# Performance work log

Measured on AMD Instinct MI355X. Metric: run time of the kernel, lower is better.

The kernel has to match this reference:

```python
import jax, jax.numpy as jnp
import numpy as np

NEG_INF = -jnp.inf

def _sage_conv(x_src, x_dst, src, dst, Wl, bl, Wr, aggr, num_nodes):
    # messages = source features gathered along edges  [E, d]
    msgs = x_src[src]
    if aggr == 'mean':
        s = jax.ops.segment_sum(msgs, dst, num_segments=num_nodes)
        cnt = jax.ops.segment_sum(jnp.ones((src.shape[0],), x_src.dtype), dst, num_segments=num_nodes)
        agg = s / jnp.maximum(cnt, 1.0)[:, None]
    else:  # max; isolated targets -> 0 (PyG scatter-max fill)
        m = jax.ops.segment_max(msgs, dst, num_segments=num_nodes)
        agg = jnp.where(jnp.isfinite(m), m, 0.0)
    return agg @ Wl.T + bl + x_dst @ Wr.T

def setup_inputs() -> dict:
    key = jax.random.key(0)
    ks = jax.random.split(key, 12)
    N, E, D, H, C, L = 40000, 640000, 128, 128, 64, 2
    sc = 0.05
    return {
        'x': jax.random.normal(ks[0], (N, D), jnp.float32),
        'edge_index0': jax.random.randint(ks[1], (2, E), 0, N, jnp.int64),
        'edge_index1': jax.random.randint(ks[2], (2, E), 0, N, jnp.int64),
        'Wl_mean': jax.random.normal(ks[3], (L, H, D), jnp.float32) * sc,
        'bl_mean': jax.random.normal(ks[4], (L, H), jnp.float32) * sc,
        'Wr_mean': jax.random.normal(ks[5], (L, H, D), jnp.float32) * sc,
        'Wl_max': jax.random.normal(ks[6], (L, H, D), jnp.float32) * sc,
        'bl_max': jax.random.normal(ks[7], (L, H), jnp.float32) * sc,
        'Wr_max': jax.random.normal(ks[8], (L, H, D), jnp.float32) * sc,
        'post_W': jax.random.normal(ks[9], (C, 2 * L * H), jnp.float32) * sc,
        'post_b': jax.random.normal(ks[10], (C,), jnp.float32) * sc,
    }

def reference(x, edge_index0, edge_index1, Wl_mean, bl_mean, Wr_mean, Wl_max, bl_max, Wr_max, post_W, post_b):
    N = x.shape[0]
    edge_sets = [edge_index0, edge_index1]
    L = len(edge_sets)
    h = x
    all_layers = []
    for i, ei in enumerate(edge_sets):
        src, dst = ei[0], ei[1]
        x_mean = _sage_conv(h, h, src, dst, Wl_mean[i], bl_mean[i], Wr_mean[i], 'mean', N)
        x_max = _sage_conv(h, h, src, dst, Wl_max[i], bl_max[i], Wr_max[i], 'max', N)
        all_layers.append(x_mean)
        all_layers.append(x_max)
        if i != L - 1:
            h = jax.nn.relu(h)  # note: original never replaces x with conv output
    x_final = jnp.concatenate(all_layers, axis=1) @ post_W.T + post_b
    return jax.nn.log_softmax(x_final, axis=-1)
```

## Files before the change

### kernel.cpp

```cpp
#include <hip/hip_runtime.h>
#include <cstdint>
#include <cstddef>

constexpr int FD = 128;
constexpr int CC = 64;
constexpr int KTOT = 768;
constexpr int CAP = 48;
constexpr int SS = 4096;

typedef __attribute__((ext_vector_type(8))) short short8;
typedef __attribute__((ext_vector_type(4))) float f32x4;

__device__ __forceinline__ float u2f(unsigned u) {
  union { unsigned u; float f; } v; v.u = u; return v.f;
}
__device__ __forceinline__ unsigned f2bf(float f) {
  union { float f; unsigned u; } v; v.f = f;
  return (v.u + 0x7FFFu + ((v.u >> 16) & 1u)) >> 16;
}
__device__ __forceinline__ unsigned pack2(float a, float b) {
  return f2bf(a) | (f2bf(b) << 16);
}
__device__ __forceinline__ unsigned relu_pk(unsigned v) {
  unsigned m = ((v >> 15) & 0x10001u) * 0xFFFFu;
  return v & ~m;
}

__global__ __launch_bounds__(256) void initpre_kernel(
    const float* __restrict__ x, uint4* __restrict__ xbf4, uint4* __restrict__ xrbf4,
    int n8, int* __restrict__ cnt, int ncnt,
    const float* __restrict__ Wl_mean, const float* __restrict__ bl_mean,
    const float* __restrict__ Wr_mean, const float* __restrict__ Wl_max,
    const float* __restrict__ bl_max,  const float* __restrict__ Wr_max,
    const float* __restrict__ postW,   const float* __restrict__ postb,
    unsigned short* __restrict__ Mbf, float* __restrict__ cb)
{
  const int gtid = blockIdx.x * 256 + threadIdx.x;
  const int gsz = gridDim.x * 256;

  for (int t = gtid; t < ncnt; t += gsz) cnt[t] = 0;

  for (int t = gtid; t < n8; t += gsz) {
    float4 a = *(const float4*)(x + (size_t)t * 8);
    float4 b = *(const float4*)(x + (size_t)t * 8 + 4);
    uint4 q;
    q.x = pack2(a.x, a.y); q.y = pack2(a.z, a.w);
    q.z = pack2(b.x, b.y); q.w = pack2(b.z, b.w);
    xbf4[t] = q;
    uint4 r;
    r.x = relu_pk(q.x); r.y = relu_pk(q.y);
    r.z = relu_pk(q.z); r.w = relu_pk(q.w);
    xrbf4[t] = r;
  }

  for (int t = gtid; t < KTOT * CC; t += gsz) {
    int c  = t & (CC - 1);
    int k  = t >> 6;
    int blk = k >> 7;
    int kk  = k & 127;
    const float* pw = postW + (size_t)c * 512;
    float acc = 0.f;
    if (blk < 4) {
      const float* W;
      if (blk == 0)      W = Wl_mean;
      else if (blk == 1) W = Wl_max;
      else if (blk == 2) W = Wl_mean + 128 * 128;
      else               W = Wl_max + 128 * 128;
      const float* pp = pw + blk * 128;
      #pragma unroll 8
      for (int h = 0; h < 128; ++h) acc += pp[h] * W[h * 128 + kk];
    } else if (blk == 4) {
      #pragma unroll 8
      for (int h = 0; h < 128; ++h)
        acc += pw[h] * Wr_mean[h * 128 + kk] + pw[128 + h] * Wr_max[h * 128 + kk];
    } else {
      const float* Wm = Wr_mean + 128 * 128;
      const float* Wx = Wr_max + 128 * 128;
      #pragma unroll 8
      for (int h = 0; h < 128; ++h)
        acc += pw[256 + h] * Wm[h * 128 + kk] + pw[384 + h] * Wx[h * 128 + kk];
    }
    Mbf[(size_t)c * KTOT + k] = (unsigned short)f2bf(acc);

    if (t < CC) {
      const float* pwc = postW + (size_t)t * 512;
      float b = postb[t];
      for (int h = 0; h < 128; ++h) {
        b += bl_mean[h]        * pwc[h]
           + bl_max[h]         * pwc[128 + h]
           + bl_mean[128 + h]  * pwc[256 + h]
           + bl_max[128 + h]   * pwc[384 + h];
      }
      cb[t] = b;
    }
  }
}

__global__ __launch_bounds__(256) void build_kernel(
    const int* __restrict__ e0, int E0,
    const int* __restrict__ e1, int E1,
    int* __restrict__ cnt, unsigned short* __restrict__ csrf, int N, int NC)
{
  const int b = blockIdx.x;
  const int c = b & 7;
  const int t = b >> 3;
  const int nst0 = (E0 + SS - 1) / SS;
  const int* e; int E; int s; int stripe;
  if (t < nst0) { e = e0; E = E0; s = 0; stripe = t; }
  else          { e = e1; E = E1; s = 1; stripe = t - nst0; }
  const int lo = c * NC;
  const int hi = min(N, lo + NC);
  const int i0 = stripe * SS;
  const int i1 = min(E, i0 + SS);
  int* mycnt = cnt + (size_t)(s * 8 + c) * NC;
  unsigned short* mycsr = csrf + (size_t)(s * 8 + c) * NC * CAP;

  for (int i = i0 + threadIdx.x; i < i1; i += 256) {
    int d = e[E + i];
    if (d >= lo && d < hi) {
      int srcv = e[i];
      int n_ = d - lo;
      int pos = atomicAdd(&mycnt[n_], 1);
      if (pos < CAP) mycsr[(size_t)pos * NC + n_] = (unsigned short)srcv;
    }
  }
}

__global__ __launch_bounds__(256) void agg_kernel(
    const unsigned* __restrict__ xbf, const unsigned* __restrict__ xrbf,
    const int* __restrict__ cnt, const unsigned short* __restrict__ csrf,
    unsigned* __restrict__ aggbf, int N, int NC)
{
  int gw = (blockIdx.x * 256 + threadIdx.x) >> 6;
  int lane = threadIdx.x & 63;
  if (gw >= 2 * N) return;
  const int layer = (gw >= N) ? 1 : 0;
  const int node = gw - layer * N;
  const int cls = node / NC;
  const int n_ = node - cls * NC;
  const int reg = layer * 8 + cls;
  const int deg = min(cnt[(size_t)reg * NC + n_], CAP);
  const char* csb = (const char*)(csrf + (size_t)reg * NC * CAP);
  const char* xl  = (const char*)(layer ? xrbf : xbf);
  const int half = lane >> 5;
  const int hl = lane & 31;
  const unsigned lb = (unsigned)hl * 8u;

  const int n0 = (deg + 1) >> 1;
  const int cbeg = half ? n0 : 0;
  const int ce   = half ? deg : n0;
  const int cnth = ce - cbeg;
  const unsigned strideB = (unsigned)NC * 2u;

  float s0 = 0.f, s1 = 0.f, s2 = 0.f, s3 = 0.f;
  float m0 = -INFINITY, m1 = -INFINITY, m2 = -INFINITY, m3 = -INFINITY;

  if (cnth > 0) {
    unsigned off = (unsigned)cbeg * strideB + (unsigned)n_ * 2u;
    const unsigned omax = (unsigned)(ce - 1) * strideB + (unsigned)n_ * 2u;
    const int niter = (cnth + 7) >> 3;
    for (int it = 0; it < niter; ++it) {
      unsigned o[8];
      #pragma unroll
      for (int u = 0; u < 8; ++u) o[u] = min(off + (unsigned)u * strideB, omax);
      off += 8u * strideB;
      unsigned idx[8];
      #pragma unroll
      for (int u = 0; u < 8; ++u) idx[u] = *(const unsigned short*)(csb + o[u]);
      uint2 g[8];
      #pragma unroll
      for (int u = 0; u < 8; ++u)
        g[u] = *(const uint2*)(xl + ((idx[u] << 8) + lb));
      #pragma unroll
      for (int u = 0; u < 8; ++u) {
        float a0 = u2f(g[u].x << 16);
        float a1 = u2f(g[u].x & 0xffff0000u);
        float a2 = u2f(g[u].y << 16);
        float a3 = u2f(g[u].y & 0xffff0000u);
        s0 += a0; s1 += a1; s2 += a2; s3 += a3;
        m0 = fmaxf(m0, a0); m1 = fmaxf(m1, a1);
        m2 = fmaxf(m2, a2); m3 = fmaxf(m3, a3);
      }
    }
    const int npad = niter * 8 - cnth;
    if (npad > 0) {
      unsigned idx = *(const unsigned short*)(csb + omax);
      uint2 g = *(const uint2*)(xl + ((idx << 8) + lb));
      float fn = (float)npad;
      s0 = fmaf(-fn, u2f(g.x << 16), s0);
      s1 = fmaf(-fn, u2f(g.x & 0xffff0000u), s1);
      s2 = fmaf(-fn, u2f(g.y << 16), s2);
      s3 = fmaf(-fn, u2f(g.y & 0xffff0000u), s3);
    }
  }

  s0 += __shfl_xor(s0, 32); s1 += __shfl_xor(s1, 32);
  s2 += __shfl_xor(s2, 32); s3 += __shfl_xor(s3, 32);
  m0 = fmaxf(m0, __shfl_xor(m0, 32)); m1 = fmaxf(m1, __shfl_xor(m1, 32));
  m2 = fmaxf(m2, __shfl_xor(m2, 32)); m3 = fmaxf(m3, __shfl_xor(m3, 32));

  if (half == 0) {
    float inv = 1.f / (float)(deg > 0 ? deg : 1);
    if (deg == 0) { m0 = 0.f; m1 = 0.f; m2 = 0.f; m3 = 0.f; }
    unsigned* am = aggbf + (size_t)(layer * 2)     * N * 64;
    unsigned* ax = aggbf + (size_t)(layer * 2 + 1) * N * 64;
    size_t o = (size_t)node * 64 + hl * 2;
    *(uint2*)(am + o) = make_uint2(pack2(s0 * inv, s1 * inv), pack2(s2 * inv, s3 * inv));
    *(uint2*)(ax + o) = make_uint2(pack2(m0, m1), pack2(m2, m3));
  }
}

__global__ __launch_bounds__(256) void gemm_kernel(
    const unsigned* __restrict__ aggbf, const unsigned* __restrict__ xbf,
    const unsigned* __restrict__ xrbf,
    const unsigned short* __restrict__ Mbf, const float* __restrict__ cb,
    float* __restrict__ out, int N)
{
  const int tid = threadIdx.x;
  const int w = tid >> 6, l = tid & 63;
  const int l15 = l & 15, lg = l >> 4;
  const int kg = lg * 8;
  const size_t N64 = (size_t)N * 64;
  const int rowb = blockIdx.x * 64 + w * 16;
  const int r0 = rowb + l15;
  const size_t a0r = (size_t)min(r0, N - 1) * 64;

  f32x4 acc[4];
  #pragma unroll
  for (int j = 0; j < 4; ++j) acc[j] = (f32x4){0.f, 0.f, 0.f, 0.f};

  #pragma unroll
  for (int b6 = 0; b6 < 6; ++b6) {
    const unsigned* Ap = (b6 < 4) ? (aggbf + (size_t)b6 * N64)
                                  : (b6 == 4 ? xbf : xrbf);
    #pragma unroll
    for (int ss = 0; ss < 4; ++ss) {
      const int k0 = b6 * 128 + ss * 32;
      const int ko = (ss * 32 + kg) >> 1;
      uint4 ua = *(const uint4*)(Ap + a0r + ko);
      short8 af = __builtin_bit_cast(short8, ua);
      #pragma unroll
      for (int fc = 0; fc < 4; ++fc) {
        const int c = fc * 16 + l15;
        uint4 qb = *(const uint4*)(Mbf + (size_t)c * KTOT + k0 + kg);
        short8 bf = __builtin_bit_cast(short8, qb);
        acc[fc] = __builtin_amdgcn_mfma_f32_16x16x32_bf16(af, bf, acc[fc], 0, 0, 0);
      }
    }
  }

  float bias[4];
  #pragma unroll
  for (int fc = 0; fc < 4; ++fc) bias[fc] = cb[fc * 16 + l15];

  #pragma unroll
  for (int i = 0; i < 4; ++i) {
    int row = rowb + lg * 4 + i;
    float z0 = acc[0][i] + bias[0];
    float z1 = acc[1][i] + bias[1];
    float z2 = acc[2][i] + bias[2];
    float z3 = acc[3][i] + bias[3];
    float m = fmaxf(fmaxf(z0, z1), fmaxf(z2, z3));
    #pragma unroll
    for (int o = 1; o < 16; o <<= 1) m = fmaxf(m, __shfl_xor(m, o));
    float s = expf(z0 - m) + expf(z1 - m) + expf(z2 - m) + expf(z3 - m);
    #pragma unroll
    for (int o = 1; o < 16; o <<= 1) s += __shfl_xor(s, o);
    float lse = m + logf(s);
    if (row < N) {
      size_t ob = (size_t)row * CC + l15;
      out[ob]      = z0 - lse;
      out[ob + 16] = z1 - lse;
      out[ob + 32] = z2 - lse;
      out[ob + 48] = z3 - lse;
    }
  }
}

extern "C" void kernel_launch(void* const* d_in, const int* in_sizes, int n_in,
                              void* d_out, int out_size, void* d_ws, size_t ws_size,
                              hipStream_t stream)
{
  const float* x       = (const float*)d_in[0];
  const int*   e0      = (const int*)d_in[1];
  const int*   e1      = (const int*)d_in[2];
  const float* Wl_mean = (const float*)d_in[3];
  const float* bl_mean = (const float*)d_in[4];
  const float* Wr_mean = (const float*)d_in[5];
  const float* Wl_max  = (const float*)d_in[6];
  const float* bl_max  = (const float*)d_in[7];
  const float* Wr_max  = (const float*)d_in[8];
  const float* postW   = (const float*)d_in[9];
  const float* postb   = (const float*)d_in[10];
  float* out = (float*)d_out;

  const int N  = in_sizes[0] / FD;
  const int E0 = in_sizes[1] / 2;
  const int E1 = in_sizes[2] / 2;
  const int NC = (N + 7) / 8;

  char* ws = (char*)d_ws;
  size_t off = 0;
  auto alloc = [&](size_t bytes) -> void* {
    void* p = ws + off;
    off = (off + bytes + 255) & ~(size_t)255;
    return p;
  };
  unsigned short* Mbf  = (unsigned short*)alloc((size_t)KTOT * CC * 2);
  float*          cbv  = (float*)alloc(CC * 4);
  int*            cnt  = (int*)alloc((size_t)16 * NC * 4);
  unsigned short* csrf = (unsigned short*)alloc((size_t)16 * NC * CAP * 2);
  unsigned*       xbf  = (unsigned*)alloc((size_t)N * 64 * 4);
  unsigned*       xrbf = (unsigned*)alloc((size_t)N * 64 * 4);
  unsigned*       aggbf= (unsigned*)alloc((size_t)4 * N * 64 * 4);
  (void)ws_size; (void)n_in; (void)out_size;

  const int n8 = N * 16;
  initpre_kernel<<<dim3(1024), dim3(256), 0, stream>>>(
      x, (uint4*)xbf, (uint4*)xrbf, n8, cnt, 16 * NC,
      Wl_mean, bl_mean, Wr_mean, Wl_max, bl_max, Wr_max, postW, postb, Mbf, cbv);

  const int nst = (E0 + SS - 1) / SS + (E1 + SS - 1) / SS;
  build_kernel<<<dim3(8 * nst), dim3(256), 0, stream>>>(
      e0, E0, e1, E1, cnt, csrf, N, NC);

  const int aggBlocks = (2 * N * 64 + 255) / 256;
  agg_kernel<<<dim3(aggBlocks), dim3(256), 0, stream>>>(
      xbf, xrbf, cnt, csrf, aggbf, N, NC);

  gemm_kernel<<<dim3((N + 63) / 64), dim3(256), 0, stream>>>(
      aggbf, xbf, xrbf, Mbf, cbv, out, N);
}
```

Measured before the change: 262.1 us.

## Merge CSR build with preprocessing kernel and pad atomic counters

Folds the edge-bucketing build step and the bf16 conversion / weight-folding step into one launch, with separate block ranges for each job, so the two independent tasks run concurrently. Counter zeroing moves to a small dedicated kernel so it finishes before the build starts. Degree counters are padded to a 16-int stride to spread atomics across cache lines, and edge destinations are read as int4 vectors. The cost is a 16x larger counter array that must be zeroed and a strided, less cache-friendly degree read in the aggregation kernel.

```diff
diff --git a/kernel.cpp b/kernel.cpp
--- a/kernel.cpp
+++ b/kernel.cpp
@@ -7,6 +7,7 @@
 constexpr int KTOT = 768;
 constexpr int CAP = 48;
 constexpr int SS = 4096;
+constexpr int CSTR = 16;
 
 typedef __attribute__((ext_vector_type(8))) short short8;
 typedef __attribute__((ext_vector_type(4))) float f32x4;
@@ -26,102 +27,121 @@
   return v & ~m;
 }
 
-__global__ __launch_bounds__(256) void initpre_kernel(
+__global__ __launch_bounds__(256) void zero_kernel(uint4* __restrict__ p, int n4) {
+  int i = blockIdx.x * 256 + threadIdx.x;
+  if (i < n4) p[i] = make_uint4(0u, 0u, 0u, 0u);
+}
+
+__global__ __launch_bounds__(256) void prebuild_kernel(
     const float* __restrict__ x, uint4* __restrict__ xbf4, uint4* __restrict__ xrbf4,
-    int n8, int* __restrict__ cnt, int ncnt,
+    int n8,
+    const int* __restrict__ e0, int E0,
+    const int* __restrict__ e1, int E1,
+    int* __restrict__ cnt, unsigned short* __restrict__ csrf, int N, int NC, int nbuild,
     const float* __restrict__ Wl_mean, const float* __restrict__ bl_mean,
     const float* __restrict__ Wr_mean, const float* __restrict__ Wl_max,
     const float* __restrict__ bl_max,  const float* __restrict__ Wr_max,
     const float* __restrict__ postW,   const float* __restrict__ postb,
     unsigned short* __restrict__ Mbf, float* __restrict__ cb)
 {
-  const int gtid = blockIdx.x * 256 + threadIdx.x;
-  const int gsz = gridDim.x * 256;
-
-  for (int t = gtid; t < ncnt; t += gsz) cnt[t] = 0;
-
-  for (int t = gtid; t < n8; t += gsz) {
-    float4 a = *(const float4*)(x + (size_t)t * 8);
-    float4 b = *(const float4*)(x + (size_t)t * 8 + 4);
-    uint4 q;
-    q.x = pack2(a.x, a.y); q.y = pack2(a.z, a.w);
-    q.z = pack2(b.x, b.y); q.w = pack2(b.z, b.w);
-    xbf4[t] = q;
-    uint4 r;
-    r.x = relu_pk(q.x); r.y = relu_pk(q.y);
-    r.z = relu_pk(q.z); r.w = relu_pk(q.w);
-    xrbf4[t] = r;
-  }
-
-  for (int t = gtid; t < KTOT * CC; t += gsz) {
-    int c  = t & (CC - 1);
-    int k  = t >> 6;
-    int blk = k >> 7;
-    int kk  = k & 127;
-    const float* pw = postW + (size_t)c * 512;
-    float acc = 0.f;
-    if (blk < 4) {
-      const float* W;
-      if (blk == 0)      W = Wl_mean;
-      else if (blk == 1) W = Wl_max;
-      else if (blk == 2) W = Wl_mean + 128 * 128;
-      else               W = Wl_max + 128 * 128;
-      const float* pp = pw + blk * 128;
-      #pragma unroll 8
-      for (int h = 0; h < 128; ++h) acc += pp[h] * W[h * 128 + kk];
-    } else if (blk == 4) {
-      #pragma unroll 8
-      for (int h = 0; h < 128; ++h)
-        acc += pw[h] * Wr_mean[h * 128 + kk] + pw[128 + h] * Wr_max[h * 128 + kk];
-    } else {
-      const float* Wm = Wr_mean + 128 * 128;
-      const float* Wx = Wr_max + 128 * 128;
-      #pragma unroll 8
-      for (int h = 0; h < 128; ++h)
-        acc += pw[256 + h] * Wm[h * 128 + kk] + pw[384 + h] * Wx[h * 128 + kk];
-    }
-    Mbf[(size_t)c * KTOT + k] = (unsigned short)f2bf(acc);
-
-    if (t < CC) {
-      const float* pwc = postW + (size_t)t * 512;
-      float b = postb[t];
-      for (int h = 0; h < 128; ++h) {
-        b += bl_mean[h]        * pwc[h]
-           + bl_max[h]         * pwc[128 + h]
-           + bl_mean[128 + h]  * pwc[256 + h]
-           + bl_max[128 + h]   * pwc[384 + h];
-      }
-      cb[t] = b;
-    }
-  }
-}
-
-__global__ __launch_bounds__(256) void build_kernel(
-    const int* __restrict__ e0, int E0,
-    const int* __restrict__ e1, int E1,
-    int* __restrict__ cnt, unsigned short* __restrict__ csrf, int N, int NC)
-{
-  const int b = blockIdx.x;
-  const int c = b & 7;
-  const int t = b >> 3;
-  const int nst0 = (E0 + SS - 1) / SS;
-  const int* e; int E; int s; int stripe;
-  if (t < nst0) { e = e0; E = E0; s = 0; stripe = t; }
-  else          { e = e1; E = E1; s = 1; stripe = t - nst0; }
-  const int lo = c * NC;
-  const int hi = min(N, lo + NC);
-  const int i0 = stripe * SS;
-  const int i1 = min(E, i0 + SS);
-  int* mycnt = cnt + (size_t)(s * 8 + c) * NC;
-  unsigned short* mycsr = csrf + (size_t)(s * 8 + c) * NC * CAP;
-
-  for (int i = i0 + threadIdx.x; i < i1; i += 256) {
-    int d = e[E + i];
-    if (d >= lo && d < hi) {
-      int srcv = e[i];
-      int n_ = d - lo;
-      int pos = atomicAdd(&mycnt[n_], 1);
-      if (pos < CAP) mycsr[(size_t)pos * NC + n_] = (unsigned short)srcv;
+  if (blockIdx.x < nbuild) {
+    const int b = blockIdx.x;
+    const int c = b & 7;
+    const int t = b >> 3;
+    const int nst0 = (E0 + SS - 1) / SS;
+    const int* e; int E; int s; int stripe;
+    if (t < nst0) { e = e0; E = E0; s = 0; stripe = t; }
+    else          { e = e1; E = E1; s = 1; stripe = t - nst0; }
+    const int lo = c * NC;
+    const int hi = min(N, lo + NC);
+    const int i0 = stripe * SS;
+    const int i1 = min(E, i0 + SS);
+    int* mycnt = cnt + (size_t)(s * 8 + c) * NC * CSTR;
+    unsigned short* mycsr = csrf + (size_t)(s * 8 + c) * NC * CAP;
+    const bool vec4 = ((E & 3) == 0);
+
+    for (int i = i0 + threadIdx.x * 4; i < i1; i += 1024) {
+      if (vec4 && i + 3 < i1) {
+        int4 d4 = *(const int4*)(e + E + i);
+        int dd[4] = {d4.x, d4.y, d4.z, d4.w};
+        #pragma unroll
+        for (int u = 0; u < 4; ++u) {
+          if (dd[u] >= lo && dd[u] < hi) {
+            int srcv = e[i + u];
+            int n_ = dd[u] - lo;
+            int pos = atomicAdd(&mycnt[n_ * CSTR], 1);
+            if (pos < CAP) mycsr[(size_t)pos * NC + n_] = (unsigned short)srcv;
+          }
+        }
+      } else {
+        for (int u = 0; u < 4 && i + u < i1; ++u) {
+          int dd = e[E + i + u];
+          if (dd >= lo && dd < hi) {
+            int srcv = e[i + u];
+            int n_ = dd - lo;
+            int pos = atomicAdd(&mycnt[n_ * CSTR], 1);
+            if (pos < CAP) mycsr[(size_t)pos * NC + n_] = (unsigned short)srcv;
+          }
+        }
+      }
+    }
+  } else {
+    const int gtid = (blockIdx.x - nbuild) * 256 + threadIdx.x;
+    const int gsz = (gridDim.x - nbuild) * 256;
+
+    for (int t = gtid; t < n8; t += gsz) {
+      float4 a = *(const float4*)(x + (size_t)t * 8);
+      float4 b = *(const float4*)(x + (size_t)t * 8 + 4);
+      uint4 q;
+      q.x = pack2(a.x, a.y); q.y = pack2(a.z, a.w);
+      q.z = pack2(b.x, b.y); q.w = pack2(b.z, b.w);
+      xbf4[t] = q;
+      uint4 r;
+      r.x = relu_pk(q.x); r.y = relu_pk(q.y);
+      r.z = relu_pk(q.z); r.w = relu_pk(q.w);
+      xrbf4[t] = r;
+    }
+
+    for (int t = gtid; t < KTOT * CC; t += gsz) {
+      int c  = t & (CC - 1);
+      int k  = t >> 6;
+      int blk = k >> 7;
+      int kk  = k & 127;
+      const float* pw = postW + (size_t)c * 512;
+      float acc = 0.f;
+      if (blk < 4) {
+        const float* W;
+        if (blk == 0)      W = Wl_mean;
+        else if (blk == 1) W = Wl_max;
+        else if (blk == 2) W = Wl_mean + 128 * 128;
+        else               W = Wl_max + 128 * 128;
+        const float* pp = pw + blk * 128;
+        #pragma unroll 8
+        for (int h = 0; h < 128; ++h) acc += pp[h] * W[h * 128 + kk];
+      } else if (blk == 4) {
+        #pragma unroll 8
+        for (int h = 0; h < 128; ++h)
+          acc += pw[h] * Wr_mean[h * 128 + kk] + pw[128 + h] * Wr_max[h * 128 + kk];
+      } else {
+        const float* Wm = Wr_mean + 128 * 128;
+        const float* Wx = Wr_max + 128 * 128;
+        #pragma unroll 8
+        for (int h = 0; h < 128; ++h)
+          acc += pw[256 + h] * Wm[h * 128 + kk] + pw[384 + h] * Wx[h * 128 + kk];
+      }
+      Mbf[(size_t)c * KTOT + k] = (unsigned short)f2bf(acc);
+
+      if (t < CC) {
+        const float* pwc = postW + (size_t)t * 512;
+        float b = postb[t];
+        for (int h = 0; h < 128; ++h) {
+          b += bl_mean[h]        * pwc[h]
+             + bl_max[h]         * pwc[128 + h]
+             + bl_mean[128 + h]  * pwc[256 + h]
+             + bl_max[128 + h]   * pwc[384 + h];
+        }
+        cb[t] = b;
+      }
     }
   }
 }
@@ -139,7 +159,7 @@
   const int cls = node / NC;
   const int n_ = node - cls * NC;
   const int reg = layer * 8 + cls;
-  const int deg = min(cnt[(size_t)reg * NC + n_], CAP);
+  const int deg = min(cnt[((size_t)reg * NC + n_) * CSTR], CAP);
   const char* csb = (const char*)(csrf + (size_t)reg * NC * CAP);
   const char* xl  = (const char*)(layer ? xrbf : xbf);
   const int half = lane >> 5;
@@ -308,21 +328,23 @@
   };
   unsigned short* Mbf  = (unsigned short*)alloc((size_t)KTOT * CC * 2);
   float*          cbv  = (float*)alloc(CC * 4);
-  int*            cnt  = (int*)alloc((size_t)16 * NC * 4);
+  int*            cnt  = (int*)alloc((size_t)16 * NC * CSTR * 4);
   unsigned short* csrf = (unsigned short*)alloc((size_t)16 * NC * CAP * 2);
   unsigned*       xbf  = (unsigned*)alloc((size_t)N * 64 * 4);
   unsigned*       xrbf = (unsigned*)alloc((size_t)N * 64 * 4);
   unsigned*       aggbf= (unsigned*)alloc((size_t)4 * N * 64 * 4);
   (void)ws_size; (void)n_in; (void)out_size;
 
+  const int cnt4 = 16 * NC * CSTR / 4;
+  zero_kernel<<<dim3((cnt4 + 255) / 256), dim3(256), 0, stream>>>((uint4*)cnt, cnt4);
+
+  const int nst = (E0 + SS - 1) / SS + (E1 + SS - 1) / SS;
+  const int nbuild = 8 * nst;
   const int n8 = N * 16;
-  initpre_kernel<<<dim3(1024), dim3(256), 0, stream>>>(
-      x, (uint4*)xbf, (uint4*)xrbf, n8, cnt, 16 * NC,
+  prebuild_kernel<<<dim3(nbuild + 1024), dim3(256), 0, stream>>>(
+      x, (uint4*)xbf, (uint4*)xrbf, n8,
+      e0, E0, e1, E1, cnt, csrf, N, NC, nbuild,
       Wl_mean, bl_mean, Wr_mean, Wl_max, bl_max, Wr_max, postW, postb, Mbf, cbv);
-
-  const int nst = (E0 + SS - 1) / SS + (E1 + SS - 1) / SS;
-  build_kernel<<<dim3(8 * nst), dim3(256), 0, stream>>>(
-      e0, E0, e1, E1, cnt, csrf, N, NC);
 
   const int aggBlocks = (2 * N * 64 + 255) / 256;
   agg_kernel<<<dim3(aggBlocks), dim3(256), 0, stream>>>(
```

Result: faster. 256.4 us (-2.2%).
